# Kernel tuning notes

Hardware: AMD Instinct MI355X
Metric: run time of the kernel (lower is better)

## Reference

```python
import jax, jax.numpy as jnp
import numpy as np

B, C, H, W = 2, 256, 48, 48
KS = 5
HEADS = 4
DH = 64
OC = HEADS * DH
SCALE = DH ** -0.5


def setup_inputs() -> dict:
    key = jax.random.key(0)
    k1, k2, k3, k4, k5 = jax.random.split(key, 5)
    kvmap1 = jax.random.normal(k1, (B, C, H, W), dtype=jnp.float32)
    qmap = jax.random.normal(k2, (B, C, H, W), dtype=jnp.float32)
    kvmap2 = jax.random.normal(k3, (B, C, H, W), dtype=jnp.float32)
    Wq = jax.random.normal(k4, (OC, C), dtype=jnp.float32) * 0.02
    Wkv = jax.random.normal(k5, (OC, C), dtype=jnp.float32) * 0.02
    return {"kvmap1": kvmap1, "qmap": qmap, "kvmap2": kvmap2, "Wq": Wq, "Wkv": Wkv}


def reference(kvmap1, qmap, kvmap2, Wq, Wkv):
    b, c, h, w = qmap.shape
    ks = KS
    pad_lo, pad_hi = ks // 2, (ks - 1) // 2
    pad = ((0, 0), (0, 0), (pad_lo, pad_hi), (pad_lo, pad_hi))
    p1 = jnp.pad(kvmap1, pad)
    p2 = jnp.pad(kvmap2, pad)
    kv = jnp.stack([p1, p2], axis=-1)  # [b, c, Hp, Wp, 2]

    # 1x1 Conv3d (pointwise over channels); note k and v share the same projection,
    # so k == v in the original module -- compute once.
    kmap = jnp.einsum('bchwl,oc->bohwl', kv, Wkv)  # [b, oc, Hp, Wp, 2]
    q = jnp.einsum('bchw,oc->bohw', qmap, Wq)      # [b, oc, h, w]

    # local windows (im2col): window flat order is (l, k1, k2), l outermost
    kw = jnp.stack(
        [kmap[:, :, i:i + h, j:j + w, :] for i in range(ks) for j in range(ks)],
        axis=-1,
    )  # [b, oc, h, w, 2, ks*ks]
    kw = kw.reshape(b, HEADS, DH, h, w, 2 * ks * ks)
    kw = kw.transpose(0, 1, 3, 4, 5, 2).reshape(b, HEADS, h * w, 2 * ks * ks, DH)

    qh = q.reshape(b, HEADS, DH, h * w).transpose(0, 1, 3, 2) * SCALE  # [b, n, x, d]
    logits = jnp.einsum('bnxd,bnxyd->bnxy', qh, kw)
    weights = jax.nn.softmax(logits, axis=-1)
    attn = jnp.einsum('bnxy,bnxyd->bnxd', weights, kw)  # v == k
    out = attn.transpose(0, 1, 3, 2).reshape(b, HEADS * DH, h, w)
    return out
```

## Files before the change

kernel.cpp:

```cpp
#include <hip/hip_runtime.h>

#define HH 48
#define WWD 48
#define CC 256
#define OCC 256
#define NPIX 2304
#define NB 2
#define NHEADS 4
#define DHEAD 64
#define SCALE 0.125f

#define TH 2
#define TW 16
#define PHR 6
#define PWC 20
#define NPOS 120
#define NTILES 72

#define SLAB ((size_t)NPIX * OCC)

typedef __attribute__((ext_vector_type(8))) short short8v;
typedef __attribute__((ext_vector_type(4))) float floatx4;

__device__ __forceinline__ unsigned short f2bf(float f) {
    union { float f; unsigned u; } v; v.f = f;
    unsigned r = v.u + 0x7FFFu + ((v.u >> 16) & 1u);
    return (unsigned short)(r >> 16);
}
__device__ __forceinline__ float bf2f(unsigned short b) {
    union { unsigned u; float f; } v; v.u = ((unsigned)b) << 16; return v.f;
}

__device__ __forceinline__ float xreduce8(float s) {
    s += __int_as_float(__builtin_amdgcn_update_dpp(
        0, __float_as_int(s), 0xB1, 0xf, 0xf, true));
    s += __int_as_float(__builtin_amdgcn_update_dpp(
        0, __float_as_int(s), 0x4E, 0xf, 0xf, true));
    s += __shfl_xor(s, 4, 64);
    return s;
}

__global__ __launch_bounds__(256) void proj_mfma(
    const float* __restrict__ Wq, const float* __restrict__ Wkv,
    const float* __restrict__ qmap, const float* __restrict__ kv1,
    const float* __restrict__ kv2, float* __restrict__ ws)
{
    __shared__ unsigned short Bs[64 * 64];

    const int z = blockIdx.z;
    const int map = z % 3;
    const int b = z / 3;
    const float* Wmat = (map == 0) ? Wq : Wkv;
    const float* X = ((map == 0) ? qmap : (map == 1) ? kv1 : kv2)
                     + (size_t)b * CC * NPIX;
    float* out = ws + ((size_t)map * NB + b) * SLAB;

    const int tid = threadIdx.x;
    const int x0 = blockIdx.x * 64;
    const int o0 = blockIdx.y * 64;
    const int lane = tid & 63;
    const int wv = tid >> 6;
    const int l15 = lane & 15;
    const int l4 = lane >> 4;
    const int kq_w = tid >> 4;
    const int xq = tid & 15;

    const float* Arow = Wmat + (size_t)(o0 + wv * 16 + l15) * CC;

    floatx4 acc[4];
#pragma unroll
    for (int nt = 0; nt < 4; ++nt) acc[nt] = (floatx4){0.f, 0.f, 0.f, 0.f};

#pragma unroll
    for (int kt = 0; kt < 4; ++kt) {
        const int k0t = kt * 64;

        float4 av0 = *reinterpret_cast<const float4*>(Arow + k0t + l4 * 8);
        float4 av1 = *reinterpret_cast<const float4*>(Arow + k0t + l4 * 8 + 4);
        float4 av2 = *reinterpret_cast<const float4*>(Arow + k0t + 32 + l4 * 8);
        float4 av3 = *reinterpret_cast<const float4*>(Arow + k0t + 32 + l4 * 8 + 4);

        float4 xv[4];
#pragma unroll
        for (int i = 0; i < 4; ++i)
            xv[i] = *reinterpret_cast<const float4*>(
                &X[(size_t)(k0t + kq_w * 4 + i) * NPIX + x0 + xq * 4]);
        {
            float xt[4][4] = {
                {xv[0].x, xv[1].x, xv[2].x, xv[3].x},
                {xv[0].y, xv[1].y, xv[2].y, xv[3].y},
                {xv[0].z, xv[1].z, xv[2].z, xv[3].z},
                {xv[0].w, xv[1].w, xv[2].w, xv[3].w}};
#pragma unroll
            for (int j = 0; j < 4; ++j) {
                const int x = xq * 4 + j;
                ushort4 u;
                u.x = f2bf(xt[j][0]); u.y = f2bf(xt[j][1]);
                u.z = f2bf(xt[j][2]); u.w = f2bf(xt[j][3]);
                *reinterpret_cast<ushort4*>(
                    (char*)Bs + x * 128 + ((kq_w ^ (x & 15)) << 3)) = u;
            }
        }
        __syncthreads();

#pragma unroll
        for (int kc = 0; kc < 2; ++kc) {
            const float4 va = (kc == 0) ? av0 : av2;
            const float4 vb = (kc == 0) ? av1 : av3;
            const float a[8] = {va.x, va.y, va.z, va.w, vb.x, vb.y, vb.z, vb.w};
            short8v ah, al;
#pragma unroll
            for (int j = 0; j < 8; ++j) {
                const unsigned short h = f2bf(a[j]);
                ah[j] = (short)h;
                al[j] = (short)f2bf(a[j] - bf2f(h));
            }
#pragma unroll
            for (int nt = 0; nt < 4; ++nt) {
                const int x = nt * 16 + l15;
                const int kq = kc * 8 + l4 * 2;
                ushort4 b0 = *reinterpret_cast<ushort4*>(
                    (char*)Bs + x * 128 + ((kq ^ l15) << 3));
                ushort4 b1 = *reinterpret_cast<ushort4*>(
                    (char*)Bs + x * 128 + (((kq + 1) ^ l15) << 3));
                short8v bh;
                bh[0] = (short)b0.x; bh[1] = (short)b0.y;
                bh[2] = (short)b0.z; bh[3] = (short)b0.w;
                bh[4] = (short)b1.x; bh[5] = (short)b1.y;
                bh[6] = (short)b1.z; bh[7] = (short)b1.w;
                acc[nt] = __builtin_amdgcn_mfma_f32_16x16x32_bf16(ah, bh, acc[nt], 0, 0, 0);
                acc[nt] = __builtin_amdgcn_mfma_f32_16x16x32_bf16(al, bh, acc[nt], 0, 0, 0);
            }
        }
        __syncthreads();
    }

#pragma unroll
    for (int nt = 0; nt < 4; ++nt) {
        const int x = nt * 16 + l15;
        float4 v = make_float4(acc[nt][0], acc[nt][1], acc[nt][2], acc[nt][3]);
        *reinterpret_cast<float4*>(
            &out[(size_t)(x0 + x) * OCC + o0 + wv * 16 + l4 * 4]) = v;
    }
}

__global__ __launch_bounds__(256) void attn_kernel(
    const float* __restrict__ ws, float* __restrict__ out)
{
    __shared__ unsigned short kp[2 * NPOS * 64];

    const int tid = threadIdx.x;
    const int bid = blockIdx.x;
    const int tile = bid % NTILES;
    const int head = (bid / NTILES) % NHEADS;
    const int b = bid / (NTILES * NHEADS);
    const int h0 = (tile / 3) * TH;
    const int w0 = (tile % 3) * TW;

    const float* qp = ws + (size_t)(0 * NB + b) * SLAB;
    const float* k1 = ws + (size_t)(1 * NB + b) * SLAB;
    const float* k2 = ws + (size_t)(2 * NB + b) * SLAB;
    const int co = head * DHEAD;

#pragma unroll
    for (int it = 0; it < 15; ++it) {
        const int i = it * 256 + tid;
        const int seg = i & 15;
        const int ps = i >> 4;
        const int l = ps >= NPOS;
        const int pos = ps - l * NPOS;
        const int pr = pos / 20, pc = pos - pr * 20;
        const int hh = h0 + pr - 2, wp = w0 + pc - 2;
        float4 v = make_float4(0.f, 0.f, 0.f, 0.f);
        if (hh >= 0 && hh < HH && wp >= 0 && wp < WWD) {
            const float* kmap = l ? k2 : k1;
            v = *reinterpret_cast<const float4*>(
                &kmap[(size_t)(hh * WWD + wp) * OCC + co + seg * 4]);
        }
        ushort4 u;
        u.x = f2bf(v.x); u.y = f2bf(v.y); u.z = f2bf(v.z); u.w = f2bf(v.w);
        *reinterpret_cast<ushort4*>(
            (char*)kp + ps * 128 + (((seg >> 1) ^ (pos & 7)) << 4)
            + (seg & 1) * 8) = u;
    }
    __syncthreads();

    const int pixl = tid >> 3;
    const int e = tid & 7;
    const int pi = pixl >> 4, pj = pixl & 15;
    const int pix = (h0 + pi) * WWD + (w0 + pj);

    float qd[8];
    {
        float4 a = *reinterpret_cast<const float4*>(
            &qp[(size_t)pix * OCC + co + e * 8]);
        float4 c = *reinterpret_cast<const float4*>(
            &qp[(size_t)pix * OCC + co + e * 8 + 4]);
        qd[0] = a.x * SCALE; qd[1] = a.y * SCALE;
        qd[2] = a.z * SCALE; qd[3] = a.w * SCALE;
        qd[4] = c.x * SCALE; qd[5] = c.y * SCALE;
        qd[6] = c.z * SCALE; qd[7] = c.w * SCALE;
    }

    float den = 0.f;
    float acc[8];
#pragma unroll
    for (int k = 0; k < 8; ++k) acc[k] = 0.f;

#pragma unroll
    for (int r = 0; r < 25; ++r) {
        const int di = r / 5, dj = r % 5;
        const int pos = (pi + di) * PWC + (pj + dj);
        const int p7 = pos & 7;
        const char* base = (char*)kp + pos * 128 + ((e ^ p7) << 4);

        short8v ku1 = *reinterpret_cast<const short8v*>(base);
        short8v ku2 = *reinterpret_cast<const short8v*>(base + NPOS * 128);

        float k1v[8], k2v[8];
#pragma unroll
        for (int k = 0; k < 8; ++k) {
            k1v[k] = bf2f((unsigned short)ku1[k]);
            k2v[k] = bf2f((unsigned short)ku2[k]);
        }

        float s1 = 0.f, s2 = 0.f;
#pragma unroll
        for (int k = 0; k < 8; ++k) {
            s1 += qd[k] * k1v[k];
            s2 += qd[k] * k2v[k];
        }
        s1 = xreduce8(s1);
        s2 = xreduce8(s2);

        const float p1 = __expf(s1);
        const float p2 = __expf(s2);
        den += p1 + p2;
#pragma unroll
        for (int k = 0; k < 8; ++k)
            acc[k] += p1 * k1v[k] + p2 * k2v[k];
    }

    const float rden = 1.f / den;

#pragma unroll
    for (int k = 0; k < 8; ++k) {
        out[((size_t)b * OCC + co + e * 8 + k) * NPIX + pix] = acc[k] * rden;
    }
}

extern "C" void kernel_launch(void* const* d_in, const int* in_sizes, int n_in,
                              void* d_out, int out_size, void* d_ws, size_t ws_size,
                              hipStream_t stream) {
    const float* kvmap1 = (const float*)d_in[0];
    const float* qmap   = (const float*)d_in[1];
    const float* kvmap2 = (const float*)d_in[2];
    const float* Wq     = (const float*)d_in[3];
    const float* Wkv    = (const float*)d_in[4];
    float* out = (float*)d_out;
    float* ws = (float*)d_ws;

    dim3 ggrid(NPIX / 64, OCC / 64, 3 * NB);
    proj_mfma<<<ggrid, 256, 0, stream>>>(Wq, Wkv, qmap, kvmap1, kvmap2, ws);

    const int nblocks = NTILES * NHEADS * NB;
    attn_kernel<<<nblocks, 256, 0, stream>>>(ws, out);
}
```

Baseline: 36.86 us.

## Store projections as bf16 and split attention windows across two threads per channel group

The projection kernel now writes its q/k outputs as bf16 instead of fp32, which halves the workspace traffic, and the attention kernel loads them directly into shared memory with no conversion. The attention block grows to 512 threads so that each of the two kv maps is handled by its own half-group, and partial sums are combined with a shuffle. The scale is folded into a log2(e) factor so exp2f can be used. Rounding q to bf16 adds some precision loss, and the split adds cross-lane reductions and lowers the per-thread work.

```diff
diff --git a/kernel.cpp b/kernel.cpp
--- a/kernel.cpp
+++ b/kernel.cpp
@@ -8,7 +8,7 @@
 #define NB 2
 #define NHEADS 4
 #define DHEAD 64
-#define SCALE 0.125f
+#define SCALE_E 0.1803368802f
 
 #define TH 2
 #define TW 16
@@ -43,7 +43,7 @@
 __global__ __launch_bounds__(256) void proj_mfma(
     const float* __restrict__ Wq, const float* __restrict__ Wkv,
     const float* __restrict__ qmap, const float* __restrict__ kv1,
-    const float* __restrict__ kv2, float* __restrict__ ws)
+    const float* __restrict__ kv2, unsigned short* __restrict__ ws)
 {
     __shared__ unsigned short Bs[64 * 64];
 
@@ -53,7 +53,7 @@
     const float* Wmat = (map == 0) ? Wq : Wkv;
     const float* X = ((map == 0) ? qmap : (map == 1) ? kv1 : kv2)
                      + (size_t)b * CC * NPIX;
-    float* out = ws + ((size_t)map * NB + b) * SLAB;
+    unsigned short* out = ws + ((size_t)map * NB + b) * SLAB;
 
     const int tid = threadIdx.x;
     const int x0 = blockIdx.x * 64;
@@ -138,16 +138,18 @@
 #pragma unroll
     for (int nt = 0; nt < 4; ++nt) {
         const int x = nt * 16 + l15;
-        float4 v = make_float4(acc[nt][0], acc[nt][1], acc[nt][2], acc[nt][3]);
-        *reinterpret_cast<float4*>(
-            &out[(size_t)(x0 + x) * OCC + o0 + wv * 16 + l4 * 4]) = v;
-    }
-}
-
-__global__ __launch_bounds__(256) void attn_kernel(
-    const float* __restrict__ ws, float* __restrict__ out)
+        ushort4 u;
+        u.x = f2bf(acc[nt][0]); u.y = f2bf(acc[nt][1]);
+        u.z = f2bf(acc[nt][2]); u.w = f2bf(acc[nt][3]);
+        *reinterpret_cast<ushort4*>(
+            &out[(size_t)(x0 + x) * OCC + o0 + wv * 16 + l4 * 4]) = u;
+    }
+}
+
+__global__ __launch_bounds__(512, 4) void attn_kernel(
+    const unsigned short* __restrict__ ws, float* __restrict__ out)
 {
-    __shared__ unsigned short kp[2 * NPOS * 64];
+    __shared__ __align__(16) unsigned short kp[2 * NPOS * 64];
 
     const int tid = threadIdx.x;
     const int bid = blockIdx.x;
@@ -157,50 +159,49 @@
     const int h0 = (tile / 3) * TH;
     const int w0 = (tile % 3) * TW;
 
-    const float* qp = ws + (size_t)(0 * NB + b) * SLAB;
-    const float* k1 = ws + (size_t)(1 * NB + b) * SLAB;
-    const float* k2 = ws + (size_t)(2 * NB + b) * SLAB;
+    const unsigned short* qp = ws + (size_t)(0 * NB + b) * SLAB;
+    const unsigned short* k1 = ws + (size_t)(1 * NB + b) * SLAB;
+    const unsigned short* k2 = ws + (size_t)(2 * NB + b) * SLAB;
     const int co = head * DHEAD;
 
 #pragma unroll
-    for (int it = 0; it < 15; ++it) {
-        const int i = it * 256 + tid;
-        const int seg = i & 15;
-        const int ps = i >> 4;
-        const int l = ps >= NPOS;
-        const int pos = ps - l * NPOS;
-        const int pr = pos / 20, pc = pos - pr * 20;
-        const int hh = h0 + pr - 2, wp = w0 + pc - 2;
-        float4 v = make_float4(0.f, 0.f, 0.f, 0.f);
-        if (hh >= 0 && hh < HH && wp >= 0 && wp < WWD) {
-            const float* kmap = l ? k2 : k1;
-            v = *reinterpret_cast<const float4*>(
-                &kmap[(size_t)(hh * WWD + wp) * OCC + co + seg * 4]);
+    for (int it = 0; it < 4; ++it) {
+        const int g = it * 512 + tid;
+        if (g < 2 * NPOS * 8) {
+            const int row = g >> 3;
+            const int u = g & 7;
+            const int lm = row >= NPOS;
+            const int pos = row - (lm ? NPOS : 0);
+            const int pr = pos / PWC, pc = pos - pr * PWC;
+            const int hh = h0 + pr - 2, wp = w0 + pc - 2;
+            short8v v = {0, 0, 0, 0, 0, 0, 0, 0};
+            if (hh >= 0 && hh < HH && wp >= 0 && wp < WWD) {
+                const unsigned short* kmap = lm ? k2 : k1;
+                v = *reinterpret_cast<const short8v*>(
+                    &kmap[(size_t)(hh * WWD + wp) * OCC + co
+                          + ((u ^ (pos & 7)) << 3)]);
+            }
+            *reinterpret_cast<short8v*>(&kp[row * 64 + u * 8]) = v;
         }
-        ushort4 u;
-        u.x = f2bf(v.x); u.y = f2bf(v.y); u.z = f2bf(v.z); u.w = f2bf(v.w);
-        *reinterpret_cast<ushort4*>(
-            (char*)kp + ps * 128 + (((seg >> 1) ^ (pos & 7)) << 4)
-            + (seg & 1) * 8) = u;
     }
     __syncthreads();
 
-    const int pixl = tid >> 3;
     const int e = tid & 7;
+    const int l = (tid >> 3) & 1;
+    const int pixl = tid >> 4;
     const int pi = pixl >> 4, pj = pixl & 15;
     const int pix = (h0 + pi) * WWD + (w0 + pj);
 
     float qd[8];
     {
-        float4 a = *reinterpret_cast<const float4*>(
+        short8v qv = *reinterpret_cast<const short8v*>(
             &qp[(size_t)pix * OCC + co + e * 8]);
-        float4 c = *reinterpret_cast<const float4*>(
-            &qp[(size_t)pix * OCC + co + e * 8 + 4]);
-        qd[0] = a.x * SCALE; qd[1] = a.y * SCALE;
-        qd[2] = a.z * SCALE; qd[3] = a.w * SCALE;
-        qd[4] = c.x * SCALE; qd[5] = c.y * SCALE;
-        qd[6] = c.z * SCALE; qd[7] = c.w * SCALE;
-    }
+#pragma unroll
+        for (int k = 0; k < 8; ++k)
+            qd[k] = bf2f((unsigned short)qv[k]) * SCALE_E;
+    }
+
+    const unsigned short* kbase = kp + l * NPOS * 64;
 
     float den = 0.f;
     float acc[8];
@@ -212,40 +213,33 @@
         const int di = r / 5, dj = r % 5;
         const int pos = (pi + di) * PWC + (pj + dj);
         const int p7 = pos & 7;
-        const char* base = (char*)kp + pos * 128 + ((e ^ p7) << 4);
-
-        short8v ku1 = *reinterpret_cast<const short8v*>(base);
-        short8v ku2 = *reinterpret_cast<const short8v*>(base + NPOS * 128);
-
-        float k1v[8], k2v[8];
-#pragma unroll
-        for (int k = 0; k < 8; ++k) {
-            k1v[k] = bf2f((unsigned short)ku1[k]);
-            k2v[k] = bf2f((unsigned short)ku2[k]);
-        }
-
-        float s1 = 0.f, s2 = 0.f;
-#pragma unroll
-        for (int k = 0; k < 8; ++k) {
-            s1 += qd[k] * k1v[k];
-            s2 += qd[k] * k2v[k];
-        }
-        s1 = xreduce8(s1);
-        s2 = xreduce8(s2);
-
-        const float p1 = __expf(s1);
-        const float p2 = __expf(s2);
-        den += p1 + p2;
-#pragma unroll
-        for (int k = 0; k < 8; ++k)
-            acc[k] += p1 * k1v[k] + p2 * k2v[k];
-    }
-
+        short8v kv = *reinterpret_cast<const short8v*>(
+            &kbase[pos * 64 + ((e ^ p7) << 3)]);
+
+        float kvf[8];
+#pragma unroll
+        for (int k = 0; k < 8; ++k) kvf[k] = bf2f((unsigned short)kv[k]);
+
+        float s = 0.f;
+#pragma unroll
+        for (int k = 0; k < 8; ++k) s += qd[k] * kvf[k];
+        s = xreduce8(s);
+
+        const float p = exp2f(s);
+        den += p;
+#pragma unroll
+        for (int k = 0; k < 8; ++k) acc[k] += p * kvf[k];
+    }
+
+    den += __shfl_xor(den, 8, 64);
+#pragma unroll
+    for (int k = 0; k < 8; ++k) acc[k] += __shfl_xor(acc[k], 8, 64);
     const float rden = 1.f / den;
 
 #pragma unroll
-    for (int k = 0; k < 8; ++k) {
-        out[((size_t)b * OCC + co + e * 8 + k) * NPIX + pix] = acc[k] * rden;
+    for (int k = 0; k < 4; ++k) {
+        const int ch = co + e * 8 + l * 4 + k;
+        out[((size_t)b * OCC + ch) * NPIX + pix] = acc[l * 4 + k] * rden;
     }
 }
 
@@ -258,11 +252,11 @@
     const float* Wq     = (const float*)d_in[3];
     const float* Wkv    = (const float*)d_in[4];
     float* out = (float*)d_out;
-    float* ws = (float*)d_ws;
+    unsigned short* ws = (unsigned short*)d_ws;
 
     dim3 ggrid(NPIX / 64, OCC / 64, 3 * NB);
     proj_mfma<<<ggrid, 256, 0, stream>>>(Wq, Wkv, qmap, kvmap1, kvmap2, ws);
 
     const int nblocks = NTILES * NHEADS * NB;
-    attn_kernel<<<nblocks, 256, 0, stream>>>(ws, out);
-}
+    attn_kernel<<<nblocks, 512, 0, stream>>>(ws, out);
+}
```

New measurement: 102.7 us. +178.6%, slower.
